# Optimization experiments

Measured on AMD Instinct MI355X. Metric: run time of the kernel, lower is better.

## Reference

```python
import jax, jax.numpy as jnp
import numpy as np

N = 50000        # nodes
E = 800000       # edges (before self-loops)
F_IN = 128       # num_features
HID = 32         # hidden_size per head
HEADS = 4
CLS = 40         # num_classes
NEG_SLOPE = 0.2  # PyG GATConv default leaky_relu slope


def setup_inputs() -> dict:
    key = jax.random.key(0)
    ks = jax.random.split(key, 10)
    s = lambda k, sh: (jax.random.normal(k, sh, jnp.float32) * 0.05)
    x = jax.random.normal(ks[0], (N, F_IN), jnp.float32)
    edge_index = jax.random.randint(ks[1], (2, E), 0, N, dtype=jnp.int64)
    W1 = s(ks[2], (F_IN, HEADS * HID))
    att_src1 = s(ks[3], (HEADS, HID))
    att_dst1 = s(ks[4], (HEADS, HID))
    b1 = jnp.zeros((HEADS * HID,), jnp.float32)
    W2 = s(ks[5], (HEADS * HID, CLS))
    att_src2 = s(ks[6], (1, CLS))
    att_dst2 = s(ks[7], (1, CLS))
    b2 = jnp.zeros((CLS,), jnp.float32)
    return {"x": x, "edge_index": edge_index, "W1": W1, "att_src1": att_src1,
            "att_dst1": att_dst1, "b1": b1, "W2": W2, "att_src2": att_src2,
            "att_dst2": att_dst2, "b2": b2}


def _add_self_loops(edge_index, num_nodes):
    ar = jnp.arange(num_nodes, dtype=edge_index.dtype)
    loops = jnp.stack([ar, ar])
    return jnp.concatenate([edge_index, loops], axis=1)


def _gat_conv(x, edge_index, W, a_src, a_dst, bias, heads, concat):
    """PyG GATConv (eval mode, additive attention, self-loops already added)."""
    n = x.shape[0]
    src, dst = edge_index[0], edge_index[1]
    h = (x @ W).reshape(n, heads, -1)                 # [N, H, C]
    a_s = jnp.einsum('nhc,hc->nh', h, a_src)          # [N, H]
    a_d = jnp.einsum('nhc,hc->nh', h, a_dst)          # [N, H]
    e = jax.nn.leaky_relu(a_s[src] + a_d[dst], NEG_SLOPE)   # [E', H]
    m = jax.ops.segment_max(e, dst, num_segments=n)   # segment softmax over dst
    ex = jnp.exp(e - m[dst])
    den = jax.ops.segment_sum(ex, dst, num_segments=n)
    alpha = ex / den[dst]                             # [E', H]
    out = jax.ops.segment_sum(h[src] * alpha[:, :, None], dst, num_segments=n)
    out = out.reshape(n, -1) if concat else out.mean(axis=1)
    return out + bias


def reference(x, edge_index, W1, att_src1, att_dst1, b1, W2, att_src2, att_dst2, b2):
    ei = _add_self_loops(edge_index, x.shape[0])
    # dropout p=0 in eval -> identity
    h = jax.nn.relu(_gat_conv(x, ei, W1, att_src1, att_dst1, b1, HEADS, True))
    out = _gat_conv(h, ei, W2, att_src2, att_dst2, b2, 1, True)  # heads=1
    return out
```

## Files before the change

### kernel.cpp

```cpp
#include <hip/hip_runtime.h>
#include <cstdint>

#define NODES 50000
#define FIN   128
#define C1    128
#define HEADS 4
#define HID   32
#define CLS   40
#define SLOPE 0.2f

#define NBUCK ((NODES + 255) >> 8)
#define EPB 2048
#define BCAP 8192

__device__ __forceinline__ float lrelu(float v) { return v > 0.f ? v : SLOPE * v; }

__device__ __forceinline__ unsigned short f2bf(float f) {
    union { float f; unsigned u; } v; v.f = f;
    unsigned u = v.u;
    return (unsigned short)((u + 0x7FFFu + ((u >> 16) & 1u)) >> 16);
}
__device__ __forceinline__ float bf2f(unsigned short b) {
    union { unsigned u; float f; } v; v.u = ((unsigned)b) << 16;
    return v.f;
}
__device__ __forceinline__ float bflo(unsigned u) {
    union { unsigned x; float f; } v; v.x = u << 16; return v.f;
}
__device__ __forceinline__ float bfhi(unsigned u) {
    union { unsigned x; float f; } v; v.x = u & 0xffff0000u; return v.f;
}

typedef __attribute__((ext_vector_type(8))) short bf16x8;
typedef __attribute__((ext_vector_type(4))) float f32x4;
typedef __attribute__((ext_vector_type(4), aligned(4))) int int4a;
typedef __attribute__((ext_vector_type(2), aligned(4))) int int2a;

__global__ __launch_bounds__(256) void k_prep(const float* __restrict__ W,
                                              unsigned short* __restrict__ w1t,
                                              int* __restrict__ bwp) {
    const int t = threadIdx.x;
#pragma unroll
    for (int i = 0; i < 64; i++) {
        int p = i * 256 + t;
        int n = p >> 7, k = p & 127;
        w1t[n * 128 + k] = f2bf(W[(size_t)k * C1 + n]);
    }
    if (t < NBUCK) bwp[t] = t * BCAP;
}

__global__ __launch_bounds__(256) void k_gemm1(const float* __restrict__ X,
                                               const unsigned short* __restrict__ w1t,
                                               const float* __restrict__ AS,
                                               const float* __restrict__ AD,
                                               unsigned short* __restrict__ h1b,
                                               float* __restrict__ as1,
                                               float* __restrict__ ad1) {
    __shared__ unsigned short Asm[64][136];
    __shared__ unsigned short Wt[128][136];
    const int t = threadIdx.x;
    const int row0 = blockIdx.x * 64;

#pragma unroll
    for (int i = 0; i < 8; i++) {
        int p = i * 256 + t;
        int n = p >> 4, k8 = (p & 15) * 8;
        *(uint4*)(&Wt[n][k8]) = *(const uint4*)(w1t + n * 128 + k8);
    }
    {
        int r = t >> 2, c0 = (t & 3) * 32;
        int gr = row0 + r;
        unsigned short tb[32];
        if (gr < NODES) {
#pragma unroll
            for (int i = 0; i < 8; i++) {
                float4 v = *(const float4*)(X + (size_t)gr * FIN + c0 + i * 4);
                tb[i * 4 + 0] = f2bf(v.x); tb[i * 4 + 1] = f2bf(v.y);
                tb[i * 4 + 2] = f2bf(v.z); tb[i * 4 + 3] = f2bf(v.w);
            }
        } else {
#pragma unroll
            for (int i = 0; i < 32; i++) tb[i] = 0;
        }
#pragma unroll
        for (int i = 0; i < 4; i++) {
            uint4 pk;
            pk.x = (unsigned)tb[i*8+0] | ((unsigned)tb[i*8+1] << 16);
            pk.y = (unsigned)tb[i*8+2] | ((unsigned)tb[i*8+3] << 16);
            pk.z = (unsigned)tb[i*8+4] | ((unsigned)tb[i*8+5] << 16);
            pk.w = (unsigned)tb[i*8+6] | ((unsigned)tb[i*8+7] << 16);
            *(uint4*)(&Asm[r][c0 + i * 8]) = pk;
        }
    }
    __syncthreads();

    const int w = t >> 6, l = t & 63;
    const int lm = l & 15, quad = l >> 4;
    f32x4 acc[8];
#pragma unroll
    for (int ct = 0; ct < 8; ct++) acc[ct] = (f32x4){0.f, 0.f, 0.f, 0.f};
#pragma unroll
    for (int kt = 0; kt < 4; kt++) {
        bf16x8 a = *(const bf16x8*)(&Asm[w * 16 + lm][kt * 32 + quad * 8]);
#pragma unroll
        for (int ct = 0; ct < 8; ct++) {
            bf16x8 b = *(const bf16x8*)(&Wt[ct * 16 + lm][kt * 32 + quad * 8]);
            acc[ct] = __builtin_amdgcn_mfma_f32_16x16x32_bf16(a, b, acc[ct], 0, 0, 0);
        }
    }
    __syncthreads();
#pragma unroll
    for (int ct = 0; ct < 8; ct++)
#pragma unroll
        for (int r = 0; r < 4; r++)
            Asm[w * 16 + quad * 4 + r][ct * 16 + lm] = f2bf(acc[ct][r]);
    __syncthreads();
    {
        int r = t >> 2, c0 = (t & 3) * 32;
        int gr = row0 + r;
        if (gr < NODES) {
#pragma unroll
            for (int i = 0; i < 4; i++)
                *(uint4*)(h1b + (size_t)gr * C1 + c0 + i * 8) =
                    *(uint4*)(&Asm[r][c0 + i * 8]);
        }
    }
    {
        int r = t >> 2, h = t & 3;
        int gr = row0 + r;
        if (gr < NODES) {
            float s = 0.f, d = 0.f;
#pragma unroll
            for (int j = 0; j < 32; j++) {
                float v = bf2f(Asm[r][h * 32 + j]);
                s = fmaf(v, AS[h * HID + j], s);
                d = fmaf(v, AD[h * HID + j], d);
            }
            as1[gr * HEADS + h] = s;
            ad1[gr * HEADS + h] = d;
        }
    }
}

__global__ __launch_bounds__(256) void k_bucketA(const int* __restrict__ src,
                                                 const int* __restrict__ dst, int E,
                                                 int* __restrict__ bwp,
                                                 int* __restrict__ tmp) {
    __shared__ int cnt[NBUCK];
    __shared__ int bbs[NBUCK];
    const int t = threadIdx.x;
    for (int i = t; i < NBUCK; i += 256) cnt[i] = 0;
    __syncthreads();
    const int e0 = blockIdx.x * EPB;
    int v[8], rb[8];
#pragma unroll
    for (int k = 0; k < 8; k++) {
        int e = e0 + k * 256 + t;
        rb[k] = -1;
        if (e < E) {
            int d = dst[e], s = src[e];
            int b = d >> 8;
            int r = atomicAdd(&cnt[b], 1);
            v[k] = (s << 8) | (d & 255);
            rb[k] = (r << 8) | b;
        }
    }
    __syncthreads();
    for (int i = t; i < NBUCK; i += 256) {
        int c = cnt[i];
        bbs[i] = c ? atomicAdd(&bwp[i], c) : 0;
    }
    __syncthreads();
#pragma unroll
    for (int k = 0; k < 8; k++) {
        if (rb[k] >= 0) {
            int b = rb[k] & 255;
            int r = rb[k] >> 8;
            tmp[bbs[b] + r] = v[k];
        }
    }
}

__global__ __launch_bounds__(256) void k_bucketB(const int* __restrict__ bwp,
                                                 const int* __restrict__ tmp,
                                                 int* __restrict__ col,
                                                 int* __restrict__ rowptr,
                                                 int* __restrict__ degarr) {
    __shared__ int degs[256];
    __shared__ int wp[256];
    __shared__ int wsum[4];
    const int b = blockIdx.x, t = threadIdx.x;
    const int n0 = b << 8;
    const int beg = b * BCAP;
    const int end = bwp[b];
    degs[t] = 0;
    __syncthreads();
    for (int e = beg + t; e < end; e += 256)
        atomicAdd(&degs[tmp[e] & 255], 1);
    __syncthreads();
    const int d = degs[t];
    int incl = d;
    const int lane = t & 63, w = t >> 6;
#pragma unroll
    for (int s = 1; s < 64; s <<= 1) {
        int u = __shfl_up(incl, s);
        if (lane >= s) incl += u;
    }
    if (lane == 63) wsum[w] = incl;
    __syncthreads();
    if (t == 0) {
        int r = 0;
#pragma unroll
        for (int i = 0; i < 4; i++) { int x = wsum[i]; wsum[i] = r; r += x; }
    }
    __syncthreads();
    const int excl = incl - d + wsum[w] + beg;
    const int nidx = n0 + t;
    if (nidx < NODES) { rowptr[nidx] = excl; degarr[nidx] = d; }
    wp[t] = excl;
    __syncthreads();
    for (int e = beg + t; e < end; e += 256) {
        int v = tmp[e];
        int p = atomicAdd(&wp[v & 255], 1);
        col[p] = v >> 8;
    }
}

__global__ __launch_bounds__(256) void k_agg1(const unsigned short* __restrict__ h1b,
                                              const float* __restrict__ as1,
                                              const float* __restrict__ ad1,
                                              const int* __restrict__ rowptr,
                                              const int* __restrict__ degarr,
                                              const int* __restrict__ col,
                                              const float* __restrict__ b1,
                                              float* __restrict__ out1) {
    int wid = (blockIdx.x * 256 + threadIdx.x) >> 6;
    if (wid >= NODES) return;
    const int lane = threadIdx.x & 63;
    const int q  = lane >> 4;
    const int ll = lane & 15;
    const int fh = ll >> 2;
    const int n = wid;
    const float adn = ad1[n * HEADS + fh];
    const int rs = rowptr[n];
    const int re = rs + degarr[n];

    float den = 0.f;
    float ac[8];
#pragma unroll
    for (int k = 0; k < 8; k++) ac[k] = 0.f;

    int base = rs;
    for (; base + 16 <= re; base += 16) {
        int4a cc = *(const int4a*)(col + base + q * 4);
        float w0 = __expf(lrelu(as1[cc.x * HEADS + fh] + adn));
        float w1 = __expf(lrelu(as1[cc.y * HEADS + fh] + adn));
        float w2 = __expf(lrelu(as1[cc.z * HEADS + fh] + adn));
        float w3 = __expf(lrelu(as1[cc.w * HEADS + fh] + adn));
        den += (w0 + w1) + (w2 + w3);
        uint4 p0 = *(const uint4*)((const char*)h1b + (((unsigned)cc.x << 8) + (unsigned)(ll << 4)));
        uint4 p1 = *(const uint4*)((const char*)h1b + (((unsigned)cc.y << 8) + (unsigned)(ll << 4)));
        uint4 p2 = *(const uint4*)((const char*)h1b + (((unsigned)cc.z << 8) + (unsigned)(ll << 4)));
        uint4 p3 = *(const uint4*)((const char*)h1b + (((unsigned)cc.w << 8) + (unsigned)(ll << 4)));
        ac[0] = fmaf(w0, bflo(p0.x), ac[0]); ac[1] = fmaf(w0, bfhi(p0.x), ac[1]);
        ac[2] = fmaf(w0, bflo(p0.y), ac[2]); ac[3] = fmaf(w0, bfhi(p0.y), ac[3]);
        ac[4] = fmaf(w0, bflo(p0.z), ac[4]); ac[5] = fmaf(w0, bfhi(p0.z), ac[5]);
        ac[6] = fmaf(w0, bflo(p0.w), ac[6]); ac[7] = fmaf(w0, bfhi(p0.w), ac[7]);
        ac[0] = fmaf(w1, bflo(p1.x), ac[0]); ac[1] = fmaf(w1, bfhi(p1.x), ac[1]);
        ac[2] = fmaf(w1, bflo(p1.y), ac[2]); ac[3] = fmaf(w1, bfhi(p1.y), ac[3]);
        ac[4] = fmaf(w1, bflo(p1.z), ac[4]); ac[5] = fmaf(w1, bfhi(p1.z), ac[5]);
        ac[6] = fmaf(w1, bflo(p1.w), ac[6]); ac[7] = fmaf(w1, bfhi(p1.w), ac[7]);
        ac[0] = fmaf(w2, bflo(p2.x), ac[0]); ac[1] = fmaf(w2, bfhi(p2.x), ac[1]);
        ac[2] = fmaf(w2, bflo(p2.y), ac[2]); ac[3] = fmaf(w2, bfhi(p2.y), ac[3]);
        ac[4] = fmaf(w2, bflo(p2.z), ac[4]); ac[5] = fmaf(w2, bfhi(p2.z), ac[5]);
        ac[6] = fmaf(w2, bflo(p2.w), ac[6]); ac[7] = fmaf(w2, bfhi(p2.w), ac[7]);
        ac[0] = fmaf(w3, bflo(p3.x), ac[0]); ac[1] = fmaf(w3, bfhi(p3.x), ac[1]);
        ac[2] = fmaf(w3, bflo(p3.y), ac[2]); ac[3] = fmaf(w3, bfhi(p3.y), ac[3]);
        ac[4] = fmaf(w3, bflo(p3.z), ac[4]); ac[5] = fmaf(w3, bfhi(p3.z), ac[5]);
        ac[6] = fmaf(w3, bflo(p3.w), ac[6]); ac[7] = fmaf(w3, bfhi(p3.w), ac[7]);
    }
    for (; base < re; base += 4) {
        int i = base + q;
        int c = (i < re) ? col[i] : n;
        float w = __expf(lrelu(as1[c * HEADS + fh] + adn));
        if (i >= re) w = 0.f;
        den += w;
        unsigned off = ((unsigned)c << 8) + (unsigned)(ll << 4);
        uint4 pk = *(const uint4*)((const char*)h1b + off);
        ac[0] = fmaf(w, bflo(pk.x), ac[0]); ac[1] = fmaf(w, bfhi(pk.x), ac[1]);
        ac[2] = fmaf(w, bflo(pk.y), ac[2]); ac[3] = fmaf(w, bfhi(pk.y), ac[3]);
        ac[4] = fmaf(w, bflo(pk.z), ac[4]); ac[5] = fmaf(w, bfhi(pk.z), ac[5]);
        ac[6] = fmaf(w, bflo(pk.w), ac[6]); ac[7] = fmaf(w, bfhi(pk.w), ac[7]);
    }
    den += __shfl_xor(den, 16);
    den += __shfl_xor(den, 32);
#pragma unroll
    for (int k = 0; k < 8; k++) {
        ac[k] += __shfl_xor(ac[k], 16);
        ac[k] += __shfl_xor(ac[k], 32);
    }
    const float wself = __expf(lrelu(as1[n * HEADS + fh] + adn));
    den += wself;
    if (q == 0) {
        unsigned offs = ((unsigned)n << 8) + (unsigned)(ll << 4);
        uint4 sp = *(const uint4*)((const char*)h1b + offs);
        float sv[8] = {bflo(sp.x), bfhi(sp.x), bflo(sp.y), bfhi(sp.y),
                       bflo(sp.z), bfhi(sp.z), bflo(sp.w), bfhi(sp.w)};
        float4 bv0 = *(const float4*)(b1 + ll * 8);
        float4 bv1 = *(const float4*)(b1 + ll * 8 + 4);
        float bb[8] = {bv0.x, bv0.y, bv0.z, bv0.w, bv1.x, bv1.y, bv1.z, bv1.w};
        float o[8];
#pragma unroll
        for (int k = 0; k < 8; k++)
            o[k] = fmaxf((ac[k] + wself * sv[k]) / den + bb[k], 0.f);
        *(float4*)(out1 + (size_t)n * C1 + ll * 8) =
            make_float4(o[0], o[1], o[2], o[3]);
        *(float4*)(out1 + (size_t)n * C1 + ll * 8 + 4) =
            make_float4(o[4], o[5], o[6], o[7]);
    }
}

__global__ __launch_bounds__(320) void k_gemm2(const float* __restrict__ A,
                                               const float* __restrict__ W,
                                               const float* __restrict__ AS,
                                               const float* __restrict__ AD,
                                               unsigned short* __restrict__ h2b,
                                               float* __restrict__ as2,
                                               float* __restrict__ ad2) {
    __shared__ float xs[64][132];
    __shared__ float ws2[128 * 40];
    __shared__ float sS[320];
    __shared__ float sD[320];
    const int tid = threadIdx.x;
    const int row0 = blockIdx.x * 64;
    for (int q = tid; q < 1280; q += 320)
        *(float4*)(ws2 + q * 4) = *(const float4*)(W + q * 4);
    for (int q = tid; q < 2048; q += 320) {
        int r = q >> 5, kq = (q & 31) * 4;
        int gr = row0 + r;
        float4 v = make_float4(0.f, 0.f, 0.f, 0.f);
        if (gr < NODES) v = *(const float4*)(A + (size_t)gr * FIN + kq);
        *(float4*)(&xs[r][kq]) = v;
    }
    __syncthreads();
    const int r = tid / 5;
    const int c0 = (tid % 5) * 8;
    float acc[8];
#pragma unroll
    for (int j = 0; j < 8; j++) acc[j] = 0.f;
    for (int k = 0; k < 128; k++) {
        float a = xs[r][k];
        float4 b0 = *(float4*)(ws2 + k * CLS + c0);
        float4 b1 = *(float4*)(ws2 + k * CLS + c0 + 4);
        acc[0] = fmaf(a, b0.x, acc[0]); acc[1] = fmaf(a, b0.y, acc[1]);
        acc[2] = fmaf(a, b0.z, acc[2]); acc[3] = fmaf(a, b0.w, acc[3]);
        acc[4] = fmaf(a, b1.x, acc[4]); acc[5] = fmaf(a, b1.y, acc[5]);
        acc[6] = fmaf(a, b1.z, acc[6]); acc[7] = fmaf(a, b1.w, acc[7]);
    }
    {
        float s = 0.f, d = 0.f;
#pragma unroll
        for (int j = 0; j < 8; j++) {
            s = fmaf(acc[j], AS[c0 + j], s);
            d = fmaf(acc[j], AD[c0 + j], d);
        }
        sS[tid] = s; sD[tid] = d;
    }
    int gr = row0 + r;
    if (gr < NODES) {
        unsigned short tb[8];
#pragma unroll
        for (int j = 0; j < 8; j++) tb[j] = f2bf(acc[j]);
        uint4 pk;
        pk.x = (unsigned)tb[0] | ((unsigned)tb[1] << 16);
        pk.y = (unsigned)tb[2] | ((unsigned)tb[3] << 16);
        pk.z = (unsigned)tb[4] | ((unsigned)tb[5] << 16);
        pk.w = (unsigned)tb[6] | ((unsigned)tb[7] << 16);
        *(uint4*)(h2b + (size_t)gr * 64 + c0) = pk;
    }
    __syncthreads();
    if (tid < 64) {
        int grr = row0 + tid;
        if (grr < NODES) {
            int b5 = tid * 5;
            as2[grr] = sS[b5] + sS[b5+1] + sS[b5+2] + sS[b5+3] + sS[b5+4];
            ad2[grr] = sD[b5] + sD[b5+1] + sD[b5+2] + sD[b5+3] + sD[b5+4];
        }
    }
}

__global__ __launch_bounds__(256) void k_agg2(const unsigned short* __restrict__ h2b,
                                              const float* __restrict__ as2,
                                              const float* __restrict__ ad2,
                                              const int* __restrict__ rowptr,
                                              const int* __restrict__ degarr,
                                              const int* __restrict__ col,
                                              const float* __restrict__ b2,
                                              float* __restrict__ out) {
    int wid = (blockIdx.x * 256 + threadIdx.x) >> 6;
    if (wid >= NODES) return;
    const int lane = threadIdx.x & 63;
    const int q8 = lane >> 3, l8 = lane & 7;
    const int n = wid;
    const float adn = ad2[n];
    const int rs = rowptr[n];
    const int re = rs + degarr[n];

    float den = 0.f;
    float ac[8];
#pragma unroll
    for (int k = 0; k < 8; k++) ac[k] = 0.f;

    int base = rs;
    for (; base + 16 <= re; base += 16) {
        int2a cc = *(const int2a*)(col + base + q8 * 2);
        float w0 = __expf(lrelu(as2[cc.x] + adn));
        float w1 = __expf(lrelu(as2[cc.y] + adn));
        den += w0 + w1;
        if (l8 < 5) {
            unsigned o0 = ((unsigned)cc.x << 7) + (unsigned)(l8 << 4);
            unsigned o1 = ((unsigned)cc.y << 7) + (unsigned)(l8 << 4);
            uint4 p0 = *(const uint4*)((const char*)h2b + o0);
            uint4 p1 = *(const uint4*)((const char*)h2b + o1);
            ac[0] = fmaf(w0, bflo(p0.x), ac[0]); ac[1] = fmaf(w0, bfhi(p0.x), ac[1]);
            ac[2] = fmaf(w0, bflo(p0.y), ac[2]); ac[3] = fmaf(w0, bfhi(p0.y), ac[3]);
            ac[4] = fmaf(w0, bflo(p0.z), ac[4]); ac[5] = fmaf(w0, bfhi(p0.z), ac[5]);
            ac[6] = fmaf(w0, bflo(p0.w), ac[6]); ac[7] = fmaf(w0, bfhi(p0.w), ac[7]);
            ac[0] = fmaf(w1, bflo(p1.x), ac[0]); ac[1] = fmaf(w1, bfhi(p1.x), ac[1]);
            ac[2] = fmaf(w1, bflo(p1.y), ac[2]); ac[3] = fmaf(w1, bfhi(p1.y), ac[3]);
            ac[4] = fmaf(w1, bflo(p1.z), ac[4]); ac[5] = fmaf(w1, bfhi(p1.z), ac[5]);
            ac[6] = fmaf(w1, bflo(p1.w), ac[6]); ac[7] = fmaf(w1, bfhi(p1.w), ac[7]);
        }
    }
    for (; base < re; base += 8) {
        int i = base + q8;
        int c = (i < re) ? col[i] : n;
        float w = __expf(lrelu(as2[c] + adn));
        if (i >= re) w = 0.f;
        den += w;
        if (l8 < 5) {
            unsigned off = ((unsigned)c << 7) + (unsigned)(l8 << 4);
            uint4 pk = *(const uint4*)((const char*)h2b + off);
            ac[0] = fmaf(w, bflo(pk.x), ac[0]); ac[1] = fmaf(w, bfhi(pk.x), ac[1]);
            ac[2] = fmaf(w, bflo(pk.y), ac[2]); ac[3] = fmaf(w, bfhi(pk.y), ac[3]);
            ac[4] = fmaf(w, bflo(pk.z), ac[4]); ac[5] = fmaf(w, bfhi(pk.z), ac[5]);
            ac[6] = fmaf(w, bflo(pk.w), ac[6]); ac[7] = fmaf(w, bfhi(pk.w), ac[7]);
        }
    }
    den += __shfl_xor(den, 8);
    den += __shfl_xor(den, 16);
    den += __shfl_xor(den, 32);
#pragma unroll
    for (int k = 0; k < 8; k++) {
        ac[k] += __shfl_xor(ac[k], 8);
        ac[k] += __shfl_xor(ac[k], 16);
        ac[k] += __shfl_xor(ac[k], 32);
    }
    const float wself = __expf(lrelu(as2[n] + adn));
    den += wself;
    if (q8 == 0 && l8 < 5) {
        unsigned offs = ((unsigned)n << 7) + (unsigned)(l8 << 4);
        uint4 sp = *(const uint4*)((const char*)h2b + offs);
        float sv[8] = {bflo(sp.x), bfhi(sp.x), bflo(sp.y), bfhi(sp.y),
                       bflo(sp.z), bfhi(sp.z), bflo(sp.w), bfhi(sp.w)};
        float4 bv0 = *(const float4*)(b2 + l8 * 8);
        float4 bv1 = *(const float4*)(b2 + l8 * 8 + 4);
        float bb[8] = {bv0.x, bv0.y, bv0.z, bv0.w, bv1.x, bv1.y, bv1.z, bv1.w};
        float o[8];
#pragma unroll
        for (int k = 0; k < 8; k++)
            o[k] = (ac[k] + wself * sv[k]) / den + bb[k];
        *(float4*)(out + (size_t)n * CLS + l8 * 8) =
            make_float4(o[0], o[1], o[2], o[3]);
        *(float4*)(out + (size_t)n * CLS + l8 * 8 + 4) =
            make_float4(o[4], o[5], o[6], o[7]);
    }
}

extern "C" void kernel_launch(void* const* d_in, const int* in_sizes, int n_in,
                              void* d_out, int out_size, void* d_ws, size_t ws_size,
                              hipStream_t stream) {
    const float* x     = (const float*)d_in[0];
    const int*   ei    = (const int*)d_in[1];
    const float* W1    = (const float*)d_in[2];
    const float* aS1   = (const float*)d_in[3];
    const float* aD1   = (const float*)d_in[4];
    const float* b1    = (const float*)d_in[5];
    const float* W2    = (const float*)d_in[6];
    const float* aS2   = (const float*)d_in[7];
    const float* aD2   = (const float*)d_in[8];
    const float* b2    = (const float*)d_in[9];
    float* out = (float*)d_out;
    const int E = in_sizes[1] / 2;
    const int* src = ei;
    const int* dst = ei + E;

    char* ws = (char*)d_ws;
    size_t off = 0;
    auto alloc = [&](size_t bytes) -> char* {
        char* p = ws + off;
        off += (bytes + 255) & ~(size_t)255;
        return p;
    };
    unsigned short* h1b = (unsigned short*)alloc((size_t)NODES * C1 * 2);
    float* out1   = (float*)alloc((size_t)NODES * C1 * 4);
    unsigned short* h2b = (unsigned short*)alloc((size_t)NODES * 64 * 2);
    float* as1    = (float*)alloc((size_t)NODES * HEADS * 4);
    float* ad1    = (float*)alloc((size_t)NODES * HEADS * 4);
    float* as2    = (float*)alloc((size_t)NODES * 4);
    float* ad2    = (float*)alloc((size_t)NODES * 4);
    int* rowptr   = (int*)alloc((size_t)NODES * 4);
    int* degarr   = (int*)alloc((size_t)NODES * 4);
    int* col      = (int*)alloc((size_t)NBUCK * BCAP * 4);
    int* tmp      = (int*)alloc((size_t)NBUCK * BCAP * 4);
    unsigned short* w1t = (unsigned short*)alloc((size_t)FIN * C1 * 2);
    int* bwp      = (int*)alloc((size_t)NBUCK * 4);

    k_prep<<<1, 256, 0, stream>>>(W1, w1t, bwp);
    k_gemm1<<<(NODES + 63) / 64, 256, 0, stream>>>(x, w1t, aS1, aD1, h1b, as1, ad1);
    k_bucketA<<<(E + EPB - 1) / EPB, 256, 0, stream>>>(src, dst, E, bwp, tmp);
    k_bucketB<<<NBUCK, 256, 0, stream>>>(bwp, tmp, col, rowptr, degarr);
    k_agg1<<<(NODES * 64) / 256, 256, 0, stream>>>(h1b, as1, ad1, rowptr, degarr, col, b1, out1);
    k_gemm2<<<(NODES + 63) / 64, 320, 0, stream>>>(out1, W2, aS2, aD2, h2b, as2, ad2);
    k_agg2<<<(NODES * 64) / 256, 256, 0, stream>>>(h2b, as2, ad2, rowptr, degarr, col, b2, out);
}
```

Before: 232.5 us.

## Store layer-1 output as bf16 and run layer-2 GEMM on MFMA

The layer-1 aggregation now writes its ReLU output in bf16 instead of fp32, which halves that intermediate's write and read traffic. The second GEMM is rewritten to use bf16 16x16x32 MFMA with a transposed, zero-padded W2 prepared in k_prep, replacing the scalar FMA loop. k_prep also builds the W1 transpose through shared memory so its stores are coalesced. The cost is extra bf16 rounding of the hidden activations and padding of 40 output columns to 48.

```diff
diff --git a/kernel.cpp b/kernel.cpp
--- a/kernel.cpp
+++ b/kernel.cpp
@@ -36,15 +36,29 @@
 typedef __attribute__((ext_vector_type(4), aligned(4))) int int4a;
 typedef __attribute__((ext_vector_type(2), aligned(4))) int int2a;
 
-__global__ __launch_bounds__(256) void k_prep(const float* __restrict__ W,
+__global__ __launch_bounds__(256) void k_prep(const float* __restrict__ W1,
+                                              const float* __restrict__ W2,
                                               unsigned short* __restrict__ w1t,
+                                              unsigned short* __restrict__ w2t,
                                               int* __restrict__ bwp) {
+    __shared__ unsigned short Tb[128][136];
     const int t = threadIdx.x;
 #pragma unroll
     for (int i = 0; i < 64; i++) {
         int p = i * 256 + t;
+        int k = p >> 7, n = p & 127;
+        Tb[n][k] = f2bf(W1[(size_t)k * C1 + n]);
+    }
+    __syncthreads();
+#pragma unroll
+    for (int i = 0; i < 8; i++) {
+        int p = i * 256 + t;
+        int n = p >> 4, k8 = (p & 15) * 8;
+        *(uint4*)(w1t + n * 128 + k8) = *(uint4*)(&Tb[n][k8]);
+    }
+    for (int p = t; p < CLS * 128; p += 256) {
         int n = p >> 7, k = p & 127;
-        w1t[n * 128 + k] = f2bf(W[(size_t)k * C1 + n]);
+        w2t[n * 128 + k] = f2bf(W2[(size_t)k * CLS + n]);
     }
     if (t < NBUCK) bwp[t] = t * BCAP;
 }
@@ -233,7 +247,7 @@
                                               const int* __restrict__ degarr,
                                               const int* __restrict__ col,
                                               const float* __restrict__ b1,
-                                              float* __restrict__ out1) {
+                                              unsigned short* __restrict__ out1) {
     int wid = (blockIdx.x * 256 + threadIdx.x) >> 6;
     if (wid >= NODES) return;
     const int lane = threadIdx.x & 63;
@@ -309,82 +323,95 @@
         float4 bv0 = *(const float4*)(b1 + ll * 8);
         float4 bv1 = *(const float4*)(b1 + ll * 8 + 4);
         float bb[8] = {bv0.x, bv0.y, bv0.z, bv0.w, bv1.x, bv1.y, bv1.z, bv1.w};
-        float o[8];
+        unsigned short ob[8];
 #pragma unroll
         for (int k = 0; k < 8; k++)
-            o[k] = fmaxf((ac[k] + wself * sv[k]) / den + bb[k], 0.f);
-        *(float4*)(out1 + (size_t)n * C1 + ll * 8) =
-            make_float4(o[0], o[1], o[2], o[3]);
-        *(float4*)(out1 + (size_t)n * C1 + ll * 8 + 4) =
-            make_float4(o[4], o[5], o[6], o[7]);
-    }
-}
-
-__global__ __launch_bounds__(320) void k_gemm2(const float* __restrict__ A,
-                                               const float* __restrict__ W,
+            ob[k] = f2bf(fmaxf((ac[k] + wself * sv[k]) / den + bb[k], 0.f));
+        uint4 pk;
+        pk.x = (unsigned)ob[0] | ((unsigned)ob[1] << 16);
+        pk.y = (unsigned)ob[2] | ((unsigned)ob[3] << 16);
+        pk.z = (unsigned)ob[4] | ((unsigned)ob[5] << 16);
+        pk.w = (unsigned)ob[6] | ((unsigned)ob[7] << 16);
+        *(uint4*)(out1 + (size_t)n * C1 + ll * 8) = pk;
+    }
+}
+
+__global__ __launch_bounds__(256) void k_gemm2(const unsigned short* __restrict__ out1b,
+                                               const unsigned short* __restrict__ w2t,
                                                const float* __restrict__ AS,
                                                const float* __restrict__ AD,
                                                unsigned short* __restrict__ h2b,
                                                float* __restrict__ as2,
                                                float* __restrict__ ad2) {
-    __shared__ float xs[64][132];
-    __shared__ float ws2[128 * 40];
-    __shared__ float sS[320];
-    __shared__ float sD[320];
-    const int tid = threadIdx.x;
+    __shared__ unsigned short Asm[64][136];
+    __shared__ unsigned short Wt2[48][136];
+    __shared__ float Cc[64][52];
+    const int t = threadIdx.x;
     const int row0 = blockIdx.x * 64;
-    for (int q = tid; q < 1280; q += 320)
-        *(float4*)(ws2 + q * 4) = *(const float4*)(W + q * 4);
-    for (int q = tid; q < 2048; q += 320) {
-        int r = q >> 5, kq = (q & 31) * 4;
+
+    for (int p = t; p < 8 * 136; p += 256) Wt2[40 + p / 136][p % 136] = 0;
+    for (int p = t; p < 640; p += 256) {
+        int n = p >> 4, k8 = (p & 15) * 8;
+        *(uint4*)(&Wt2[n][k8]) = *(const uint4*)(w2t + n * 128 + k8);
+    }
+    {
+        int r = t >> 2, c0 = (t & 3) * 32;
         int gr = row0 + r;
-        float4 v = make_float4(0.f, 0.f, 0.f, 0.f);
-        if (gr < NODES) v = *(const float4*)(A + (size_t)gr * FIN + kq);
-        *(float4*)(&xs[r][kq]) = v;
-    }
-    __syncthreads();
-    const int r = tid / 5;
-    const int c0 = (tid % 5) * 8;
-    float acc[8];
-#pragma unroll
-    for (int j = 0; j < 8; j++) acc[j] = 0.f;
-    for (int k = 0; k < 128; k++) {
-        float a = xs[r][k];
-        float4 b0 = *(float4*)(ws2 + k * CLS + c0);
-        float4 b1 = *(float4*)(ws2 + k * CLS + c0 + 4);
-        acc[0] = fmaf(a, b0.x, acc[0]); acc[1] = fmaf(a, b0.y, acc[1]);
-        acc[2] = fmaf(a, b0.z, acc[2]); acc[3] = fmaf(a, b0.w, acc[3]);
-        acc[4] = fmaf(a, b1.x, acc[4]); acc[5] = fmaf(a, b1.y, acc[5]);
-        acc[6] = fmaf(a, b1.z, acc[6]); acc[7] = fmaf(a, b1.w, acc[7]);
-    }
+        if (gr < NODES) {
+#pragma unroll
+            for (int i = 0; i < 4; i++)
+                *(uint4*)(&Asm[r][c0 + i * 8]) =
+                    *(const uint4*)(out1b + (size_t)gr * C1 + c0 + i * 8);
+        } else {
+            uint4 z = make_uint4(0, 0, 0, 0);
+#pragma unroll
+            for (int i = 0; i < 4; i++) *(uint4*)(&Asm[r][c0 + i * 8]) = z;
+        }
+    }
+    __syncthreads();
+
+    const int w = t >> 6, l = t & 63;
+    const int lm = l & 15, quad = l >> 4;
+    f32x4 acc[3];
+#pragma unroll
+    for (int ct = 0; ct < 3; ct++) acc[ct] = (f32x4){0.f, 0.f, 0.f, 0.f};
+#pragma unroll
+    for (int kt = 0; kt < 4; kt++) {
+        bf16x8 a = *(const bf16x8*)(&Asm[w * 16 + lm][kt * 32 + quad * 8]);
+#pragma unroll
+        for (int ct = 0; ct < 3; ct++) {
+            bf16x8 b = *(const bf16x8*)(&Wt2[ct * 16 + lm][kt * 32 + quad * 8]);
+            acc[ct] = __builtin_amdgcn_mfma_f32_16x16x32_bf16(a, b, acc[ct], 0, 0, 0);
+        }
+    }
+    __syncthreads();
+#pragma unroll
+    for (int ct = 0; ct < 3; ct++)
+#pragma unroll
+        for (int r = 0; r < 4; r++)
+            Cc[w * 16 + quad * 4 + r][ct * 16 + lm] = acc[ct][r];
+    __syncthreads();
     {
-        float s = 0.f, d = 0.f;
-#pragma unroll
-        for (int j = 0; j < 8; j++) {
-            s = fmaf(acc[j], AS[c0 + j], s);
-            d = fmaf(acc[j], AD[c0 + j], d);
-        }
-        sS[tid] = s; sD[tid] = d;
-    }
-    int gr = row0 + r;
-    if (gr < NODES) {
-        unsigned short tb[8];
-#pragma unroll
-        for (int j = 0; j < 8; j++) tb[j] = f2bf(acc[j]);
-        uint4 pk;
-        pk.x = (unsigned)tb[0] | ((unsigned)tb[1] << 16);
-        pk.y = (unsigned)tb[2] | ((unsigned)tb[3] << 16);
-        pk.z = (unsigned)tb[4] | ((unsigned)tb[5] << 16);
-        pk.w = (unsigned)tb[6] | ((unsigned)tb[7] << 16);
-        *(uint4*)(h2b + (size_t)gr * 64 + c0) = pk;
-    }
-    __syncthreads();
-    if (tid < 64) {
-        int grr = row0 + tid;
-        if (grr < NODES) {
-            int b5 = tid * 5;
-            as2[grr] = sS[b5] + sS[b5+1] + sS[b5+2] + sS[b5+3] + sS[b5+4];
-            ad2[grr] = sD[b5] + sD[b5+1] + sD[b5+2] + sD[b5+3] + sD[b5+4];
+        int r = t >> 2, c0 = (t & 3) * 10;
+        int gr = row0 + r;
+        if (gr < NODES) {
+#pragma unroll
+            for (int i = 0; i < 5; i++) {
+                int c = c0 + i * 2;
+                unsigned pk = (unsigned)f2bf(Cc[r][c]) |
+                              ((unsigned)f2bf(Cc[r][c + 1]) << 16);
+                *(unsigned*)(h2b + (size_t)gr * 64 + c) = pk;
+            }
+            float s = 0.f, d = 0.f;
+#pragma unroll
+            for (int j = 0; j < 10; j++) {
+                float v = Cc[r][c0 + j];
+                s = fmaf(v, AS[c0 + j], s);
+                d = fmaf(v, AD[c0 + j], d);
+            }
+            s += __shfl_xor(s, 1); s += __shfl_xor(s, 2);
+            d += __shfl_xor(d, 1); d += __shfl_xor(d, 2);
+            if ((t & 3) == 0) { as2[gr] = s; ad2[gr] = d; }
         }
     }
 }
@@ -502,9 +529,9 @@
         off += (bytes + 255) & ~(size_t)255;
         return p;
     };
-    unsigned short* h1b = (unsigned short*)alloc((size_t)NODES * C1 * 2);
-    float* out1   = (float*)alloc((size_t)NODES * C1 * 4);
-    unsigned short* h2b = (unsigned short*)alloc((size_t)NODES * 64 * 2);
+    unsigned short* h1b  = (unsigned short*)alloc((size_t)NODES * C1 * 2);
+    unsigned short* out1 = (unsigned short*)alloc((size_t)NODES * C1 * 2);
+    unsigned short* h2b  = (unsigned short*)alloc((size_t)NODES * 64 * 2);
     float* as1    = (float*)alloc((size_t)NODES * HEADS * 4);
     float* ad1    = (float*)alloc((size_t)NODES * HEADS * 4);
     float* as2    = (float*)alloc((size_t)NODES * 4);
@@ -514,13 +541,14 @@
     int* col      = (int*)alloc((size_t)NBUCK * BCAP * 4);
     int* tmp      = (int*)alloc((size_t)NBUCK * BCAP * 4);
     unsigned short* w1t = (unsigned short*)alloc((size_t)FIN * C1 * 2);
+    unsigned short* w2t = (unsigned short*)alloc((size_t)CLS * 128 * 2);
     int* bwp      = (int*)alloc((size_t)NBUCK * 4);
 
-    k_prep<<<1, 256, 0, stream>>>(W1, w1t, bwp);
+    k_prep<<<1, 256, 0, stream>>>(W1, W2, w1t, w2t, bwp);
     k_gemm1<<<(NODES + 63) / 64, 256, 0, stream>>>(x, w1t, aS1, aD1, h1b, as1, ad1);
     k_bucketA<<<(E + EPB - 1) / EPB, 256, 0, stream>>>(src, dst, E, bwp, tmp);
     k_bucketB<<<NBUCK, 256, 0, stream>>>(bwp, tmp, col, rowptr, degarr);
     k_agg1<<<(NODES * 64) / 256, 256, 0, stream>>>(h1b, as1, ad1, rowptr, degarr, col, b1, out1);
-    k_gemm2<<<(NODES + 63) / 64, 320, 0, stream>>>(out1, W2, aS2, aD2, h2b, as2, ad2);
+    k_gemm2<<<(NODES + 63) / 64, 256, 0, stream>>>(out1, w2t, aS2, aD2, h2b, as2, ad2);
     k_agg2<<<(NODES * 64) / 256, 256, 0, stream>>>(h2b, as2, ad2, rowptr, degarr, col, b2, out);
 }
```

New measurement: 211.9 us. -8.8%, faster.
